# Kernel tuning notes

Measured on AMD Instinct MI355X. Metric: run time of the kernel, lower is better.

## Reference

```python
import jax, jax.numpy as jnp
import numpy as np
from jax import lax

T, D, H, O = 16384, 257, 512, 257


def setup_inputs() -> dict:
    key = jax.random.key(0)
    ks = jax.random.split(key, 7)
    s = 1.0 / np.sqrt(H)  # PyTorch LSTM/Linear uniform init scale
    u = lambda k, shp: jax.random.uniform(k, shp, jnp.float32, -s, s)
    return {
        "stft": jax.random.normal(ks[0], (T, D), jnp.float32),
        "W_ih": u(ks[1], (4 * H, D)),
        "W_hh": u(ks[2], (4 * H, H)),
        "b_ih": u(ks[3], (4 * H,)),
        "b_hh": u(ks[4], (4 * H,)),
        "W_out": u(ks[5], (O, H)),
        "b_out": u(ks[6], (O,)),
    }


def reference(stft, W_ih, W_hh, b_ih, b_hh, W_out, b_out):
    # Batch size is 1 (stft.view(T, 1, -1)), so we scan over [T, D] directly.
    # Precompute input-to-gate GEMM for all timesteps: [T, 4H]
    x_gates = stft @ W_ih.T + (b_ih + b_hh)

    def step(carry, xg):
        h, c = carry  # [H], [H]
        g = xg + h @ W_hh.T  # [4H], PyTorch gate order: i, f, g, o
        i, f, gg, o = jnp.split(g, 4)
        i = jax.nn.sigmoid(i)
        f = jax.nn.sigmoid(f)
        gg = jnp.tanh(gg)
        o = jax.nn.sigmoid(o)
        c = f * c + i * gg
        h = o * jnp.tanh(c)
        return (h, c), h

    h0 = jnp.zeros((H,), stft.dtype)  # init_hidden(): zeros
    c0 = jnp.zeros((H,), stft.dtype)
    _, hs = lax.scan(step, (h0, c0), x_gates)  # hs: [T, H]

    out_space = hs @ W_out.T + b_out  # [T, O]
    return jax.nn.log_softmax(out_space, axis=1)
```

## Files before the change

kernel.cpp:

```cpp
#include <hip/hip_runtime.h>
#include <cmath>

#define T_STEPS 16384
#define D_IN    257
#define H_DIM   512
#define O_DIM   257
#define G4      2048

typedef unsigned long long u64;

#define WS_XG_OFF     8192
#define WS_HS_OFF     (8192 + (size_t)T_STEPS * G4 * 4)

__device__ inline float fast_sigmoid(float x) {
    return 1.f / (1.f + __expf(-x));
}
__device__ inline float fast_tanh(float x) {
    float ax = fminf(fabsf(x), 15.f);
    float e  = __expf(2.f * ax);
    float t  = (e - 1.f) / (e + 1.f);
    return copysignf(t, x);
}

__global__ __launch_bounds__(256) void xgate_gemm(
    const float* __restrict__ stft, const float* __restrict__ W_ih,
    const float* __restrict__ b_ih, const float* __restrict__ b_hh,
    float* __restrict__ xg)
{
    const int tid = threadIdx.x;
    const int tx = tid & 15, ty = tid >> 4;
    const int j0 = blockIdx.x * 64;
    const int t0 = blockIdx.y * 64;

    __shared__ float s_a[64][17];
    __shared__ float s_b[64][17];

    float acc[4][4] = {};

    for (int k0 = 0; k0 < D_IN; k0 += 16) {
        #pragma unroll
        for (int l = 0; l < 4; ++l) {
            int idx = tid + l * 256;
            int r  = idx >> 4;
            int kk = idx & 15;
            int k  = k0 + kk;
            s_a[r][kk] = (k < D_IN) ? stft[(size_t)(t0 + r) * D_IN + k] : 0.f;
            s_b[r][kk] = (k < D_IN) ? W_ih[(size_t)(j0 + r) * D_IN + k] : 0.f;
        }
        __syncthreads();
        #pragma unroll
        for (int kk = 0; kk < 16; ++kk) {
            float a[4], b[4];
            #pragma unroll
            for (int r = 0; r < 4; ++r) a[r] = s_a[ty * 4 + r][kk];
            #pragma unroll
            for (int c = 0; c < 4; ++c) b[c] = s_b[tx * 4 + c][kk];
            #pragma unroll
            for (int r = 0; r < 4; ++r)
                #pragma unroll
                for (int c = 0; c < 4; ++c)
                    acc[r][c] += a[r] * b[c];
        }
        __syncthreads();
    }

    float bias[4];
    #pragma unroll
    for (int c = 0; c < 4; ++c) {
        int j = j0 + tx * 4 + c;
        bias[c] = b_ih[j] + b_hh[j];
    }
    #pragma unroll
    for (int r = 0; r < 4; ++r) {
        int t = t0 + ty * 4 + r;
        #pragma unroll
        for (int c = 0; c < 4; ++c) {
            xg[(size_t)t * G4 + j0 + tx * 4 + c] = acc[r][c] + bias[c];
        }
    }
}

__global__ __launch_bounds__(512, 1) void lstm_seq(
    const float* __restrict__ W_hh, const float* __restrict__ xg,
    float* __restrict__ hs, u64* msg)
{
    const int tid  = threadIdx.x;
    const int g    = blockIdx.x;
    const int w    = tid >> 6;
    const int lane = tid & 63;
    const int j    = lane & 15;
    const int gate = lane >> 4;
    const int row  = gate * H_DIM + g * 16 + j;

    float4 wv[16];
    {
        const float4* wr = (const float4*)(W_hh + (size_t)row * H_DIM + w * 64);
        #pragma unroll
        for (int i = 0; i < 16; ++i) wv[i] = wr[i];
    }

    __shared__ float s_h[512];
    __shared__ float s_part[2][512];

    u64* slot0 = msg;
    u64* slot1 = msg + 512;

    float c_state = 0.f;

    for (int t = 0; t < T_STEPS; ++t) {
        const unsigned tagt = (unsigned)t;

        float xv = 0.f;
        if (w == 0) xv = xg[(size_t)t * G4 + row];

        u64* rp = ((t & 1) ? slot1 : slot0) + tid;
        u64 u;
        for (;;) {
            u = __hip_atomic_load(rp, __ATOMIC_RELAXED, __HIP_MEMORY_SCOPE_AGENT);
            if ((unsigned)(u >> 32) == tagt) break;
        }

        s_h[tid] = __uint_as_float((unsigned)u);

        const float4* hv = (const float4*)(s_h + w * 64);
        float acc = 0.f;
        #pragma unroll
        for (int i = 0; i < 16; ++i) {
            float4 h4 = hv[i];
            acc += wv[i].x * h4.x + wv[i].y * h4.y +
                   wv[i].z * h4.z + wv[i].w * h4.w;
        }
        s_part[t & 1][tid] = acc;

        asm volatile("s_waitcnt lgkmcnt(0)\n\ts_barrier" ::: "memory");

        if (w == 0) {
            const float* pp = &s_part[t & 1][0];
            float sum = xv;
            #pragma unroll
            for (int k = 0; k < 8; ++k) sum += pp[k * 64 + lane];

            float gi = __shfl(sum, j + 0,  64);
            float gf = __shfl(sum, j + 16, 64);
            float gg = __shfl(sum, j + 32, 64);
            float go = __shfl(sum, j + 48, 64);

            float iv = fast_sigmoid(gi);
            float fv = fast_sigmoid(gf);
            float ov = fast_sigmoid(go);
            float gv = fast_tanh(gg);
            c_state = fv * c_state + iv * gv;
            float hn = ov * fast_tanh(c_state);

            if (lane < 16) {
                hs[(size_t)t * H_DIM + g * 16 + lane] = hn;
                u64 m = ((u64)(tagt + 1) << 32) | (u64)__float_as_uint(hn);
                u64* wp = (((t + 1) & 1) ? slot1 : slot0) + (g * 16 + lane);
                __hip_atomic_store(wp, m, __ATOMIC_RELAXED, __HIP_MEMORY_SCOPE_AGENT);
            }
        }
    }
}

__global__ __launch_bounds__(256) void out_softmax(
    const float* __restrict__ hs, const float* __restrict__ W_out,
    const float* __restrict__ b_out, float* __restrict__ out)
{
    const int tid = threadIdx.x;
    const int t0  = blockIdx.x * 16;

    __shared__ float s_w[257 * 33];
    __shared__ float s_hs[16 * 33];
    __shared__ float s_o[16 * 257];
    __shared__ float s_red[8];

    float acc[16] = {};
    float acc256 = 0.f;

    for (int k0 = 0; k0 < H_DIM; k0 += 32) {
        for (int idx = tid; idx < 257 * 32; idx += 256) {
            int row = idx >> 5, col = idx & 31;
            s_w[row * 33 + col] = W_out[(size_t)row * H_DIM + k0 + col];
        }
        for (int idx = tid; idx < 16 * 32; idx += 256) {
            int row = idx >> 5, col = idx & 31;
            s_hs[row * 33 + col] = hs[(size_t)(t0 + row) * H_DIM + k0 + col];
        }
        __syncthreads();
        #pragma unroll
        for (int kk = 0; kk < 32; ++kk) {
            float w = s_w[tid * 33 + kk];
            #pragma unroll
            for (int r = 0; r < 16; ++r)
                acc[r] += s_hs[r * 33 + kk] * w;
        }
        if (tid < 16) {
            #pragma unroll
            for (int kk = 0; kk < 32; ++kk)
                acc256 += s_w[256 * 33 + kk] * s_hs[tid * 33 + kk];
        }
        __syncthreads();
    }

    float bias_c = b_out[tid];
    #pragma unroll
    for (int r = 0; r < 16; ++r) s_o[r * 257 + tid] = acc[r] + bias_c;
    if (tid < 16) s_o[tid * 257 + 256] = acc256 + b_out[256];
    __syncthreads();

    const int lane = tid & 63, wid = tid >> 6;
    for (int r = 0; r < 16; ++r) {
        float v  = s_o[r * 257 + tid];
        float vx = (tid == 0) ? s_o[r * 257 + 256] : -INFINITY;
        float m = fmaxf(v, vx);
        #pragma unroll
        for (int off = 32; off > 0; off >>= 1) m = fmaxf(m, __shfl_xor(m, off, 64));
        if (lane == 0) s_red[wid] = m;
        __syncthreads();
        m = fmaxf(fmaxf(s_red[0], s_red[1]), fmaxf(s_red[2], s_red[3]));
        float e = expf(v - m) + ((tid == 0) ? expf(vx - m) : 0.f);
        #pragma unroll
        for (int off = 32; off > 0; off >>= 1) e += __shfl_xor(e, off, 64);
        if (lane == 0) s_red[4 + wid] = e;
        __syncthreads();
        float s = s_red[4] + s_red[5] + s_red[6] + s_red[7];
        float lg = logf(s) + m;
        out[(size_t)(t0 + r) * O_DIM + tid] = v - lg;
        if (tid == 0) out[(size_t)(t0 + r) * O_DIM + 256] = vx - lg;
    }
}

extern "C" void kernel_launch(void* const* d_in, const int* in_sizes, int n_in,
                              void* d_out, int out_size, void* d_ws, size_t ws_size,
                              hipStream_t stream) {
    (void)in_sizes; (void)n_in; (void)out_size; (void)ws_size;

    const float* stft  = (const float*)d_in[0];
    const float* W_ih  = (const float*)d_in[1];
    const float* W_hh  = (const float*)d_in[2];
    const float* b_ih  = (const float*)d_in[3];
    const float* b_hh  = (const float*)d_in[4];
    const float* W_out = (const float*)d_in[5];
    const float* b_out = (const float*)d_in[6];
    float* out = (float*)d_out;

    char* ws = (char*)d_ws;
    u64* msg  = (u64*)ws;
    float* xg = (float*)(ws + WS_XG_OFF);
    float* hs = (float*)(ws + WS_HS_OFF);

    (void)hipMemsetAsync(ws, 0, 8192, stream);

    xgate_gemm<<<dim3(G4 / 64, T_STEPS / 64), 256, 0, stream>>>(
        stft, W_ih, b_ih, b_hh, xg);
    lstm_seq<<<32, 512, 0, stream>>>(W_hh, xg, hs, msg);
    out_softmax<<<T_STEPS / 16, 256, 0, stream>>>(hs, W_out, b_out, out);
}
```

Before: 27.31 ms.

## Repartition LSTM recurrence across 64 blocks with per-wave hidden units and shuffle reduction

The recurrent kernel now runs on 64 blocks instead of 32, and each wave owns one hidden unit. Each lane dot-products a 32-element chunk of h against the four gate rows. Partial sums are reduced with cross-lane shuffles, which removes the second shared-memory partial-sum pass and the single-wave gate epilogue. Both the barrier before the dot product and the software-pipelined polling load are meant to shorten the per-step critical path. In exchange, the flag exchange spans more blocks and every wave runs the redundant activation math.

```diff
diff --git a/kernel.cpp b/kernel.cpp
--- a/kernel.cpp
+++ b/kernel.cpp
@@ -84,80 +84,81 @@
     const float* __restrict__ W_hh, const float* __restrict__ xg,
     float* __restrict__ hs, u64* msg)
 {
-    const int tid  = threadIdx.x;
-    const int g    = blockIdx.x;
-    const int w    = tid >> 6;
-    const int lane = tid & 63;
-    const int j    = lane & 15;
-    const int gate = lane >> 4;
-    const int row  = gate * H_DIM + g * 16 + j;
-
-    float4 wv[16];
+    const int tid   = threadIdx.x;
+    const int b     = blockIdx.x;
+    const int w     = tid >> 6;
+    const int lane  = tid & 63;
+    const int gate  = lane >> 4;
+    const int chunk = lane & 15;
+    const int hglob = b * 8 + w;
+    const int row   = gate * H_DIM + hglob;
+
+    float4 wv[8];
     {
-        const float4* wr = (const float4*)(W_hh + (size_t)row * H_DIM + w * 64);
-        #pragma unroll
-        for (int i = 0; i < 16; ++i) wv[i] = wr[i];
-    }
-
-    __shared__ float s_h[512];
-    __shared__ float s_part[2][512];
+        const float4* wr = (const float4*)(W_hh + (size_t)row * H_DIM + chunk * 32);
+        #pragma unroll
+        for (int i = 0; i < 8; ++i) wv[i] = wr[i];
+    }
+
+    __shared__ float s_h[2][16 * 36];
 
     u64* slot0 = msg;
     u64* slot1 = msg + 512;
 
     float c_state = 0.f;
 
+    const int sa = (tid >> 5) * 36 + (tid & 31);
+
     for (int t = 0; t < T_STEPS; ++t) {
         const unsigned tagt = (unsigned)t;
 
-        float xv = 0.f;
-        if (w == 0) xv = xg[(size_t)t * G4 + row];
+        float xv = __builtin_nontemporal_load(xg + (size_t)t * G4 + row);
 
         u64* rp = ((t & 1) ? slot1 : slot0) + tid;
-        u64 u;
+        u64 a = __hip_atomic_load(rp, __ATOMIC_RELAXED, __HIP_MEMORY_SCOPE_AGENT);
+        u64 n = __hip_atomic_load(rp, __ATOMIC_RELAXED, __HIP_MEMORY_SCOPE_AGENT);
         for (;;) {
-            u = __hip_atomic_load(rp, __ATOMIC_RELAXED, __HIP_MEMORY_SCOPE_AGENT);
-            if ((unsigned)(u >> 32) == tagt) break;
-        }
-
-        s_h[tid] = __uint_as_float((unsigned)u);
-
-        const float4* hv = (const float4*)(s_h + w * 64);
+            if ((unsigned)(a >> 32) == tagt) break;
+            a = n;
+            n = __hip_atomic_load(rp, __ATOMIC_RELAXED, __HIP_MEMORY_SCOPE_AGENT);
+        }
+
+        s_h[t & 1][sa] = __uint_as_float((unsigned)a);
+
+        asm volatile("s_waitcnt lgkmcnt(0)\n\ts_barrier" ::: "memory");
+
+        const float4* hv = (const float4*)(&s_h[t & 1][chunk * 36]);
         float acc = 0.f;
         #pragma unroll
-        for (int i = 0; i < 16; ++i) {
+        for (int i = 0; i < 8; ++i) {
             float4 h4 = hv[i];
             acc += wv[i].x * h4.x + wv[i].y * h4.y +
                    wv[i].z * h4.z + wv[i].w * h4.w;
         }
-        s_part[t & 1][tid] = acc;
-
-        asm volatile("s_waitcnt lgkmcnt(0)\n\ts_barrier" ::: "memory");
-
-        if (w == 0) {
-            const float* pp = &s_part[t & 1][0];
-            float sum = xv;
-            #pragma unroll
-            for (int k = 0; k < 8; ++k) sum += pp[k * 64 + lane];
-
-            float gi = __shfl(sum, j + 0,  64);
-            float gf = __shfl(sum, j + 16, 64);
-            float gg = __shfl(sum, j + 32, 64);
-            float go = __shfl(sum, j + 48, 64);
-
-            float iv = fast_sigmoid(gi);
-            float fv = fast_sigmoid(gf);
-            float ov = fast_sigmoid(go);
-            float gv = fast_tanh(gg);
-            c_state = fv * c_state + iv * gv;
-            float hn = ov * fast_tanh(c_state);
-
-            if (lane < 16) {
-                hs[(size_t)t * H_DIM + g * 16 + lane] = hn;
-                u64 m = ((u64)(tagt + 1) << 32) | (u64)__float_as_uint(hn);
-                u64* wp = (((t + 1) & 1) ? slot1 : slot0) + (g * 16 + lane);
-                __hip_atomic_store(wp, m, __ATOMIC_RELAXED, __HIP_MEMORY_SCOPE_AGENT);
-            }
+
+        acc += __shfl_xor(acc, 1, 64);
+        acc += __shfl_xor(acc, 2, 64);
+        acc += __shfl_xor(acc, 4, 64);
+        acc += __shfl_xor(acc, 8, 64);
+        float total = acc + xv;
+
+        float gi = __shfl(total, 0,  64);
+        float gf = __shfl(total, 16, 64);
+        float gg = __shfl(total, 32, 64);
+        float go = __shfl(total, 48, 64);
+
+        float iv = fast_sigmoid(gi);
+        float fv = fast_sigmoid(gf);
+        float ov = fast_sigmoid(go);
+        float gv = fast_tanh(gg);
+        c_state = fv * c_state + iv * gv;
+        float hn = ov * fast_tanh(c_state);
+
+        if (lane == 0) {
+            __builtin_nontemporal_store(hn, hs + (size_t)t * H_DIM + hglob);
+            u64 m = ((u64)(tagt + 1) << 32) | (u64)__float_as_uint(hn);
+            u64* wp = (((t + 1) & 1) ? slot1 : slot0) + hglob;
+            __hip_atomic_store(wp, m, __ATOMIC_RELAXED, __HIP_MEMORY_SCOPE_AGENT);
         }
     }
 }
@@ -253,6 +254,6 @@
 
     xgate_gemm<<<dim3(G4 / 64, T_STEPS / 64), 256, 0, stream>>>(
         stft, W_ih, b_ih, b_hh, xg);
-    lstm_seq<<<32, 512, 0, stream>>>(W_hh, xg, hs, msg);
+    lstm_seq<<<64, 512, 0, stream>>>(W_hh, xg, hs, msg);
     out_softmax<<<T_STEPS / 16, 256, 0, stream>>>(hs, W_out, b_out, out);
 }
```

Result: slower. 52.62 ms (+92.7%).

## Remap LSTM recurrent matvec so lanes share h loads across four gates

Applied to the files above, without the earlier changes.

Each lane now holds a 16-column slice of W_hh for all four gate rows of one hidden unit, instead of a 64-column slice of a single gate row. Each thread therefore reads only 16 h values from shared memory rather than 64, and the four partial dot products are reduced with a butterfly of xor-shuffles. The goal is to cut LDS reads per step on the latency-bound sequential recurrence, at the cost of extra cross-lane shuffles.

```diff
diff --git a/kernel.cpp b/kernel.cpp
--- a/kernel.cpp
+++ b/kernel.cpp
@@ -20,6 +20,9 @@
     float e  = __expf(2.f * ax);
     float t  = (e - 1.f) / (e + 1.f);
     return copysignf(t, x);
+}
+__device__ inline float dot4(float4 a, float4 b) {
+    return a.x * b.x + a.y * b.y + a.z * b.z + a.w * b.w;
 }
 
 __global__ __launch_bounds__(256) void xgate_gemm(
@@ -88,15 +91,23 @@
     const int g    = blockIdx.x;
     const int w    = tid >> 6;
     const int lane = tid & 63;
-    const int j    = lane & 15;
-    const int gate = lane >> 4;
-    const int row  = gate * H_DIM + g * 16 + j;
-
-    float4 wv[16];
+    const int j    = lane >> 2;
+    const int c    = lane & 3;
+    const int colb = w * 64 + c * 16;
+
+    const float* wbase = W_hh + (size_t)(g * 16 + j) * H_DIM + colb;
+    const size_t gstride = (size_t)H_DIM * H_DIM;
+    float4 wA0, wA1, wA2, wA3, wB0, wB1, wB2, wB3;
+    float4 wC0, wC1, wC2, wC3, wD0, wD1, wD2, wD3;
     {
-        const float4* wr = (const float4*)(W_hh + (size_t)row * H_DIM + w * 64);
-        #pragma unroll
-        for (int i = 0; i < 16; ++i) wv[i] = wr[i];
+        const float4* p0 = (const float4*)(wbase);
+        const float4* p1 = (const float4*)(wbase + gstride);
+        const float4* p2 = (const float4*)(wbase + 2 * gstride);
+        const float4* p3 = (const float4*)(wbase + 3 * gstride);
+        wA0 = p0[0]; wA1 = p0[1]; wA2 = p0[2]; wA3 = p0[3];
+        wB0 = p1[0]; wB1 = p1[1]; wB2 = p1[2]; wB3 = p1[3];
+        wC0 = p2[0]; wC1 = p2[1]; wC2 = p2[2]; wC3 = p2[3];
+        wD0 = p3[0]; wD1 = p3[1]; wD2 = p3[2]; wD3 = p3[3];
     }
 
     __shared__ float s_h[512];
@@ -107,11 +118,13 @@
 
     float c_state = 0.f;
 
+    const int t_j    = lane & 15;
+
     for (int t = 0; t < T_STEPS; ++t) {
         const unsigned tagt = (unsigned)t;
 
         float xv = 0.f;
-        if (w == 0) xv = xg[(size_t)t * G4 + row];
+        if (w == 0) xv = xg[(size_t)t * G4 + (lane >> 4) * H_DIM + g * 16 + t_j];
 
         u64* rp = ((t & 1) ? slot1 : slot0) + tid;
         u64 u;
@@ -122,15 +135,21 @@
 
         s_h[tid] = __uint_as_float((unsigned)u);
 
-        const float4* hv = (const float4*)(s_h + w * 64);
-        float acc = 0.f;
-        #pragma unroll
-        for (int i = 0; i < 16; ++i) {
-            float4 h4 = hv[i];
-            acc += wv[i].x * h4.x + wv[i].y * h4.y +
-                   wv[i].z * h4.z + wv[i].w * h4.w;
-        }
-        s_part[t & 1][tid] = acc;
+        const float4* hv = (const float4*)(s_h + colb);
+        float4 h0 = hv[0], h1 = hv[1], h2 = hv[2], h3 = hv[3];
+
+        float p0 = dot4(wA0, h0) + dot4(wA1, h1) + dot4(wA2, h2) + dot4(wA3, h3);
+        float p1 = dot4(wB0, h0) + dot4(wB1, h1) + dot4(wB2, h2) + dot4(wB3, h3);
+        float p2 = dot4(wC0, h0) + dot4(wC1, h1) + dot4(wC2, h2) + dot4(wC3, h3);
+        float p3 = dot4(wD0, h0) + dot4(wD1, h1) + dot4(wD2, h2) + dot4(wD3, h3);
+
+        const bool lo2 = (c < 2);
+        float a0 = (lo2 ? p0 : p2) + __shfl_xor(lo2 ? p2 : p0, 2, 64);
+        float a1 = (lo2 ? p1 : p3) + __shfl_xor(lo2 ? p3 : p1, 2, 64);
+        const bool ev = ((c & 1) == 0);
+        float fin = (ev ? a0 : a1) + __shfl_xor(ev ? a1 : a0, 1, 64);
+
+        s_part[t & 1][w * 64 + c * 16 + j] = fin;
 
         asm volatile("s_waitcnt lgkmcnt(0)\n\ts_barrier" ::: "memory");
 
@@ -140,10 +159,10 @@
             #pragma unroll
             for (int k = 0; k < 8; ++k) sum += pp[k * 64 + lane];
 
-            float gi = __shfl(sum, j + 0,  64);
-            float gf = __shfl(sum, j + 16, 64);
-            float gg = __shfl(sum, j + 32, 64);
-            float go = __shfl(sum, j + 48, 64);
+            float gi = __shfl(sum, t_j + 0,  64);
+            float gf = __shfl(sum, t_j + 16, 64);
+            float gg = __shfl(sum, t_j + 32, 64);
+            float go = __shfl(sum, t_j + 48, 64);
 
             float iv = fast_sigmoid(gi);
             float fv = fast_sigmoid(gf);
```

Result: no change. 27.47 ms (+0.6%).

## Make each LSTM wavefront independent, removing block barrier and shared partial reduction

Applied to the files above, without the earlier changes.

Restructures the recurrent kernel so each wavefront owns two hidden units across all four gates, loads the full h vector itself by polling all 512 message slots, and reduces its dot products with lane shuffles instead of a shared-memory partial sum and block barrier. This removes the per-step s_barrier and the single-wavefront serial tail. The hs output is now written by one rotating block from the gathered messages rather than by every producer, with a final drain for the last step. The cost is eight times more global polling traffic per wavefront.

```diff
diff --git a/kernel.cpp b/kernel.cpp
--- a/kernel.cpp
+++ b/kernel.cpp
@@ -21,6 +21,11 @@
     float t  = (e - 1.f) / (e + 1.f);
     return copysignf(t, x);
 }
+__device__ inline float dot4(float4 a, float4 b) {
+    return a.x * b.x + a.y * b.y + a.z * b.z + a.w * b.w;
+}
+
+#define PIN4(v) asm volatile("" : "+v"(v.x), "+v"(v.y), "+v"(v.z), "+v"(v.w))
 
 __global__ __launch_bounds__(256) void xgate_gemm(
     const float* __restrict__ stft, const float* __restrict__ W_ih,
@@ -82,83 +87,129 @@
 
 __global__ __launch_bounds__(512, 1) void lstm_seq(
     const float* __restrict__ W_hh, const float* __restrict__ xg,
-    float* __restrict__ hs, u64* msg)
+    float* __restrict__ hs, u64* __restrict__ msg)
 {
     const int tid  = threadIdx.x;
     const int g    = blockIdx.x;
     const int w    = tid >> 6;
     const int lane = tid & 63;
-    const int j    = lane & 15;
-    const int gate = lane >> 4;
-    const int row  = gate * H_DIM + g * 16 + j;
+    const int rgrp = lane >> 3;
+    const int cchk = lane & 7;
+    const int par  = lane & 1;
+    const int hw   = g * 16 + 2 * w;
 
     float4 wv[16];
     {
-        const float4* wr = (const float4*)(W_hh + (size_t)row * H_DIM + w * 64);
+        const int grow = (rgrp >> 1) * H_DIM + hw + (rgrp & 1);
+        const float4* wr = (const float4*)(W_hh + (size_t)grow * H_DIM + cchk * 64);
         #pragma unroll
         for (int i = 0; i < 16; ++i) wv[i] = wr[i];
     }
 
-    __shared__ float s_h[512];
-    __shared__ float s_part[2][512];
-
-    u64* slot0 = msg;
-    u64* slot1 = msg + 512;
+    __shared__ float s_h[8][2][8 * 68];
 
     float c_state = 0.f;
 
     for (int t = 0; t < T_STEPS; ++t) {
+        const int slot = t & 1;
         const unsigned tagt = (unsigned)t;
 
-        float xv = 0.f;
-        if (w == 0) xv = xg[(size_t)t * G4 + row];
-
-        u64* rp = ((t & 1) ? slot1 : slot0) + tid;
-        u64 u;
+        const float* xp = xg + (size_t)t * G4 + hw + par;
+        float xq0 = xp[0];
+        float xq1 = xp[H_DIM];
+        float xq2 = xp[2 * H_DIM];
+        float xq3 = xp[3 * H_DIM];
+
+        u64* bp = msg + slot * 512 + lane;
+        u64 v0, v1, v2, v3, v4, v5, v6, v7;
         for (;;) {
-            u = __hip_atomic_load(rp, __ATOMIC_RELAXED, __HIP_MEMORY_SCOPE_AGENT);
-            if ((unsigned)(u >> 32) == tagt) break;
-        }
-
-        s_h[tid] = __uint_as_float((unsigned)u);
-
-        const float4* hv = (const float4*)(s_h + w * 64);
+            v0 = __hip_atomic_load(bp,       __ATOMIC_RELAXED, __HIP_MEMORY_SCOPE_AGENT);
+            v1 = __hip_atomic_load(bp + 64,  __ATOMIC_RELAXED, __HIP_MEMORY_SCOPE_AGENT);
+            v2 = __hip_atomic_load(bp + 128, __ATOMIC_RELAXED, __HIP_MEMORY_SCOPE_AGENT);
+            v3 = __hip_atomic_load(bp + 192, __ATOMIC_RELAXED, __HIP_MEMORY_SCOPE_AGENT);
+            v4 = __hip_atomic_load(bp + 256, __ATOMIC_RELAXED, __HIP_MEMORY_SCOPE_AGENT);
+            v5 = __hip_atomic_load(bp + 320, __ATOMIC_RELAXED, __HIP_MEMORY_SCOPE_AGENT);
+            v6 = __hip_atomic_load(bp + 384, __ATOMIC_RELAXED, __HIP_MEMORY_SCOPE_AGENT);
+            v7 = __hip_atomic_load(bp + 448, __ATOMIC_RELAXED, __HIP_MEMORY_SCOPE_AGENT);
+            if ((unsigned)(v0 >> 32) == tagt && (unsigned)(v1 >> 32) == tagt &&
+                (unsigned)(v2 >> 32) == tagt && (unsigned)(v3 >> 32) == tagt &&
+                (unsigned)(v4 >> 32) == tagt && (unsigned)(v5 >> 32) == tagt &&
+                (unsigned)(v6 >> 32) == tagt && (unsigned)(v7 >> 32) == tagt) break;
+        }
+
+        float* sh = &s_h[w][slot][0];
+        sh[0 * 68 + lane] = __uint_as_float((unsigned)v0);
+        sh[1 * 68 + lane] = __uint_as_float((unsigned)v1);
+        sh[2 * 68 + lane] = __uint_as_float((unsigned)v2);
+        sh[3 * 68 + lane] = __uint_as_float((unsigned)v3);
+        sh[4 * 68 + lane] = __uint_as_float((unsigned)v4);
+        sh[5 * 68 + lane] = __uint_as_float((unsigned)v5);
+        sh[6 * 68 + lane] = __uint_as_float((unsigned)v6);
+        sh[7 * 68 + lane] = __uint_as_float((unsigned)v7);
+
+        if (w == 0 && t > 0 && g == ((t - 1) & 31)) {
+            float* hp = hs + (size_t)(t - 1) * H_DIM + lane;
+            __builtin_nontemporal_store(__uint_as_float((unsigned)v0), hp);
+            __builtin_nontemporal_store(__uint_as_float((unsigned)v1), hp + 64);
+            __builtin_nontemporal_store(__uint_as_float((unsigned)v2), hp + 128);
+            __builtin_nontemporal_store(__uint_as_float((unsigned)v3), hp + 192);
+            __builtin_nontemporal_store(__uint_as_float((unsigned)v4), hp + 256);
+            __builtin_nontemporal_store(__uint_as_float((unsigned)v5), hp + 320);
+            __builtin_nontemporal_store(__uint_as_float((unsigned)v6), hp + 384);
+            __builtin_nontemporal_store(__uint_as_float((unsigned)v7), hp + 448);
+        }
+
+        PIN4(wv[0]);  PIN4(wv[1]);  PIN4(wv[2]);  PIN4(wv[3]);
+        PIN4(wv[4]);  PIN4(wv[5]);  PIN4(wv[6]);  PIN4(wv[7]);
+        PIN4(wv[8]);  PIN4(wv[9]);  PIN4(wv[10]); PIN4(wv[11]);
+        PIN4(wv[12]); PIN4(wv[13]); PIN4(wv[14]); PIN4(wv[15]);
+
+        const float4* hv = (const float4*)(sh + 68 * cchk);
         float acc = 0.f;
         #pragma unroll
-        for (int i = 0; i < 16; ++i) {
-            float4 h4 = hv[i];
-            acc += wv[i].x * h4.x + wv[i].y * h4.y +
-                   wv[i].z * h4.z + wv[i].w * h4.w;
-        }
-        s_part[t & 1][tid] = acc;
-
-        asm volatile("s_waitcnt lgkmcnt(0)\n\ts_barrier" ::: "memory");
-
-        if (w == 0) {
-            const float* pp = &s_part[t & 1][0];
-            float sum = xv;
-            #pragma unroll
-            for (int k = 0; k < 8; ++k) sum += pp[k * 64 + lane];
-
-            float gi = __shfl(sum, j + 0,  64);
-            float gf = __shfl(sum, j + 16, 64);
-            float gg = __shfl(sum, j + 32, 64);
-            float go = __shfl(sum, j + 48, 64);
-
-            float iv = fast_sigmoid(gi);
-            float fv = fast_sigmoid(gf);
-            float ov = fast_sigmoid(go);
-            float gv = fast_tanh(gg);
-            c_state = fv * c_state + iv * gv;
-            float hn = ov * fast_tanh(c_state);
-
-            if (lane < 16) {
-                hs[(size_t)t * H_DIM + g * 16 + lane] = hn;
-                u64 m = ((u64)(tagt + 1) << 32) | (u64)__float_as_uint(hn);
-                u64* wp = (((t + 1) & 1) ? slot1 : slot0) + (g * 16 + lane);
-                __hip_atomic_store(wp, m, __ATOMIC_RELAXED, __HIP_MEMORY_SCOPE_AGENT);
+        for (int i = 0; i < 16; ++i) acc += dot4(wv[i], hv[i]);
+
+        acc += __shfl_xor(acc, 1, 64);
+        acc += __shfl_xor(acc, 2, 64);
+        acc += __shfl_xor(acc, 4, 64);
+
+        float S0 = __shfl(acc, (0 + par) * 8, 64) + xq0;
+        float S1 = __shfl(acc, (2 + par) * 8, 64) + xq1;
+        float S2 = __shfl(acc, (4 + par) * 8, 64) + xq2;
+        float S3 = __shfl(acc, (6 + par) * 8, 64) + xq3;
+
+        float iv = fast_sigmoid(S0);
+        float fv = fast_sigmoid(S1);
+        float gv = fast_tanh(S2);
+        float ov = fast_sigmoid(S3);
+        c_state = fv * c_state + iv * gv;
+        float hn = ov * fast_tanh(c_state);
+
+        if (lane < 2) {
+            u64 m = ((u64)(tagt + 1) << 32) | (u64)__float_as_uint(hn);
+            __hip_atomic_store(msg + ((t + 1) & 1) * 512 + hw + lane, m,
+                               __ATOMIC_RELAXED, __HIP_MEMORY_SCOPE_AGENT);
+        }
+    }
+
+    if (g == 31 && w == 0) {
+        u64* bp = msg + ((T_STEPS & 1) ? 512 : 0) + lane;
+        const unsigned tagT = (unsigned)T_STEPS;
+        u64 v[8];
+        for (;;) {
+            bool ok = true;
+            #pragma unroll
+            for (int k = 0; k < 8; ++k) {
+                v[k] = __hip_atomic_load(bp + k * 64, __ATOMIC_RELAXED,
+                                         __HIP_MEMORY_SCOPE_AGENT);
+                ok &= ((unsigned)(v[k] >> 32) == tagT);
             }
-        }
+            if (ok) break;
+        }
+        float* hp = hs + (size_t)(T_STEPS - 1) * H_DIM + lane;
+        #pragma unroll
+        for (int k = 0; k < 8; ++k)
+            __builtin_nontemporal_store(__uint_as_float((unsigned)v[k]), hp + k * 64);
     }
 }
 
```

Measured after the change: 72.63 ms. +166.0%, slower.
